# Performance work log

Measured on AMD Instinct MI355X. Metric: run time of the kernel, lower is better.

Reference implementation:

```python
import jax, jax.numpy as jnp
import numpy as np

N_HEAD = 16
D_HEAD = 64
MAX_REL = 512  # max_relative_positions


def setup_inputs() -> dict:
    key = jax.random.key(0)
    ks = jax.random.split(key, 9)
    B, S, D = 2, 2048, 1024
    return {
        "hidden_states": jax.random.normal(ks[0], (B, S, D), jnp.float32),
        "Wq": jax.random.normal(ks[1], (D, D), jnp.float32) * 0.02,
        "bq": jnp.zeros((D,), jnp.float32),
        "Wk": jax.random.normal(ks[2], (D, D), jnp.float32) * 0.02,
        "bk": jnp.zeros((D,), jnp.float32),
        "Wv": jax.random.normal(ks[3], (D, D), jnp.float32) * 0.02,
        "bv": jnp.zeros((D,), jnp.float32),
        "Wc": jax.random.normal(ks[4], (D, D), jnp.float32) * 0.02,
        "pos_table": jax.random.normal(ks[5], (2 * MAX_REL, D_HEAD), jnp.float32) * 0.02,
    }


def reference(hidden_states, Wq, bq, Wk, bk, Wv, bv, Wc, pos_table):
    B, S, D = hidden_states.shape
    H, Dh = N_HEAD, D_HEAD

    # QKV projections (torch Linear: x @ W.T + b)
    q = hidden_states @ Wq.T + bq
    k = hidden_states @ Wk.T + bk
    v = hidden_states @ Wv.T + bv
    q = q.reshape(B, S, H, Dh).transpose(0, 2, 1, 3)  # b h s d
    k = k.reshape(B, S, H, Dh).transpose(0, 2, 1, 3)
    v = v.reshape(B, S, H, Dh).transpose(0, 2, 1, 3)

    # relative position embedding lookup: [S, S, Dh]
    ar = jnp.arange(S)
    rel = jnp.clip(ar[:, None] - ar[None, :] + MAX_REL, 0, 2 * MAX_REL - 1)
    rpe = pos_table[rel]  # (S, S, Dh)

    # c2p: original einsum 'bhld,ijd->bhij' sums q over l (faithful)
    c2p = jnp.einsum('bhld,ijd->bhij', q, rpe)
    p2c = jnp.einsum('bhjd,ijd->bhij', k, jnp.flip(rpe, axis=0))
    bias = c2p + p2c  # (B, H, S, S)

    # SDPA with explicit attn_mask == bias added to scaled scores
    scale = 1.0 / jnp.sqrt(jnp.asarray(Dh, hidden_states.dtype))
    scores = jnp.einsum('bhid,bhjd->bhij', q, k) * scale + bias
    attn = jax.nn.softmax(scores, axis=-1)
    out = jnp.einsum('bhij,bhjd->bhid', attn, v)  # (B, H, S, Dh)

    out = out.transpose(0, 2, 1, 3).reshape(B, S, D)
    return out @ Wc.T  # c_proj has no bias; dropout is identity in eval
```

## Files before the change

kernel.cpp:

```cpp
#include <hip/hip_runtime.h>
#include <math.h>

#define BN   2
#define SEQ  2048
#define DIM  1024
#define NH   16
#define DH   64
#define TAB  1024
#define SCALE 0.125f
#define LOG2E 1.44269504088896340736f

typedef __attribute__((ext_vector_type(8))) short bf16x8;
typedef __attribute__((ext_vector_type(4))) float f32x4;

#if defined(__has_builtin)
#if __has_builtin(__builtin_amdgcn_exp2f)
#define EXP2F(x) __builtin_amdgcn_exp2f(x)
#else
#define EXP2F(x) exp2f(x)
#endif
#else
#define EXP2F(x) exp2f(x)
#endif

__device__ __forceinline__ short f2b(float f) {
    union { float f; unsigned u; } x; x.f = f;
    return (short)((x.u + 0x7fffu + ((x.u >> 16) & 1u)) >> 16);
}
__device__ __forceinline__ float b2f(short s) {
    union { float f; unsigned u; } x; x.u = ((unsigned)(unsigned short)s) << 16;
    return x.f;
}

#define GLDS16(gp, lp) __builtin_amdgcn_global_load_lds( \
    (const __attribute__((address_space(1))) void*)(gp), \
    (__attribute__((address_space(3))) void*)(lp), 16, 0, 0)

__device__ __forceinline__ bf16x8 fragS(const short* base, int row, int kq) {
    return *(const bf16x8*)(base + row * 64 + ((kq ^ (row & 7)) << 3));
}

__global__ __launch_bounds__(256) void f2b_multi_kernel(
    const float* __restrict__ s0, short* __restrict__ d0, int n0,
    const float* __restrict__ s1, short* __restrict__ d1,
    const float* __restrict__ s2, short* __restrict__ d2,
    const float* __restrict__ s3, short* __restrict__ d3, int nw,
    const float* __restrict__ s4, short* __restrict__ d4, int n4)
{
    const int z = blockIdx.z;
    const float* src = z == 0 ? s0 : (z == 1 ? s1 : (z == 2 ? s2 : (z == 3 ? s3 : s4)));
    short* dst       = z == 0 ? d0 : (z == 1 ? d1 : (z == 2 ? d2 : (z == 3 ? d3 : d4)));
    const int n      = z == 0 ? n0 : (z == 4 ? n4 : nw);
    int i = (blockIdx.x * 256 + threadIdx.x) * 8;
    if (i >= n) return;
    float4 a = *(const float4*)&src[i];
    float4 b = *(const float4*)&src[i + 4];
    bf16x8 o = { f2b(a.x), f2b(a.y), f2b(a.z), f2b(a.w),
                 f2b(b.x), f2b(b.y), f2b(b.z), f2b(b.w) };
    *(bf16x8*)&dst[i] = o;
}

__global__ __launch_bounds__(256) void qkv_mfma_kernel(
    const short* __restrict__ xb,
    const short* __restrict__ Wqb, const float* __restrict__ bq,
    const short* __restrict__ Wkb, const float* __restrict__ bk,
    const short* __restrict__ Wvb, const float* __restrict__ bv,
    short* __restrict__ q, short* __restrict__ k, short* __restrict__ v)
{
    const int which = blockIdx.z;
    const short* W    = which == 0 ? Wqb : (which == 1 ? Wkb : Wvb);
    const float* bias = which == 0 ? bq  : (which == 1 ? bk  : bv);
    short* outp       = which == 0 ? q   : (which == 1 ? k   : v);
    const float osc   = which == 0 ? SCALE * LOG2E : 1.0f;

    const int m0 = blockIdx.y * 128;
    const int n0 = blockIdx.x * 128;

    __shared__ short As[128 * 64];
    __shared__ short Bs[128 * 64];

    const int t  = threadIdx.x;
    const int w  = t >> 6;
    const int q4 = (t >> 4) & 3;
    const int l  = t & 15;
    const int wm = (w >> 1) * 64;
    const int wn = (w & 1) * 64;

    f32x4 acc[4][4];
#pragma unroll
    for (int mt = 0; mt < 4; ++mt)
#pragma unroll
        for (int nt = 0; nt < 4; ++nt) acc[mt][nt] = (f32x4){0.f,0.f,0.f,0.f};

    for (int k0 = 0; k0 < DIM; k0 += 64) {
        __syncthreads();
#pragma unroll
        for (int p = 0; p < 4; ++p) {
            const int cq = p * 256 + t;
            const int row = cq >> 3, bd = cq & 7;
            const int goff = (bd ^ (row & 7)) << 3;
            GLDS16(xb + (size_t)(m0 + row) * DIM + k0 + goff, As + cq * 8);
            GLDS16(W  + (size_t)(n0 + row) * DIM + k0 + goff, Bs + cq * 8);
        }
        __syncthreads();
#pragma unroll
        for (int kc = 0; kc < 2; ++kc) {
            bf16x8 af[4], bf[4];
#pragma unroll
            for (int mt = 0; mt < 4; ++mt) af[mt] = fragS(As, wm + mt*16 + l, kc*4 + q4);
#pragma unroll
            for (int nt = 0; nt < 4; ++nt) bf[nt] = fragS(Bs, wn + nt*16 + l, kc*4 + q4);
#pragma unroll
            for (int mt = 0; mt < 4; ++mt)
#pragma unroll
                for (int nt = 0; nt < 4; ++nt)
                    acc[mt][nt] = __builtin_amdgcn_mfma_f32_16x16x32_bf16(
                        af[mt], bf[nt], acc[mt][nt], 0, 0, 0);
        }
    }

    float bv4[4];
#pragma unroll
    for (int nt = 0; nt < 4; ++nt) bv4[nt] = bias[n0 + wn + nt*16 + l];
#pragma unroll
    for (int mt = 0; mt < 4; ++mt) {
#pragma unroll
        for (int r = 0; r < 4; ++r) {
            const int m  = m0 + wm + mt*16 + q4*4 + r;
            const int b_ = m >> 11, s_ = m & 2047;
#pragma unroll
            for (int nt = 0; nt < 4; ++nt) {
                const int o  = n0 + wn + nt*16 + l;
                const int h_ = o >> 6, d_ = o & 63;
                outp[((size_t)(b_*NH + h_) * SEQ + s_) * DH + d_] =
                    f2b((acc[mt][nt][r] + bv4[nt]) * osc);
            }
        }
    }
}

__global__ __launch_bounds__(256) void qsum_c2p_kernel(
    const short* __restrict__ q, const float* __restrict__ pt, float* __restrict__ c2p)
{
    const int bh = blockIdx.x;
    const short* qb = q + (size_t)bh * SEQ * DH;
    __shared__ float part[32][72];
    __shared__ float qs[64];
    const int t = threadIdx.x;
    const int dg = t & 7, sc = t >> 3;
    float a[8];
#pragma unroll
    for (int c = 0; c < 8; ++c) a[c] = 0.f;
    for (int s = sc * 64; s < sc * 64 + 64; ++s) {
        bf16x8 vv = *(const bf16x8*)&qb[(size_t)s * DH + dg * 8];
#pragma unroll
        for (int c = 0; c < 8; ++c) a[c] += b2f(vv[c]);
    }
#pragma unroll
    for (int c = 0; c < 8; ++c) part[sc][dg*8 + c] = a[c];
    __syncthreads();
    if (t < 64) {
        float s = 0.f;
#pragma unroll 8
        for (int i = 0; i < 32; ++i) s += part[i][t];
        qs[t] = s * 8.0f;
    }
    __syncthreads();
    for (int c = t; c < TAB; c += 256) {
        const float* ptr = pt + (size_t)c * DH;
        float s = 0.f;
#pragma unroll
        for (int dd = 0; dd < DH; dd += 4) {
            float4 p4 = *(const float4*)&ptr[dd];
            s += qs[dd]*p4.x + qs[dd+1]*p4.y + qs[dd+2]*p4.z + qs[dd+3]*p4.w;
        }
        c2p[(size_t)bh * TAB + c] = s;
    }
}

__global__ __launch_bounds__(256) void tgemm_kernel(
    const short* __restrict__ kglob, const short* __restrict__ ptb,
    short* __restrict__ slab, int bh0)
{
    const int G    = gridDim.z;
    const int gsub = G >> 3;
    const int fid  = (blockIdx.z * gridDim.y + blockIdx.y) * gridDim.x + blockIdx.x;
    const int g    = (fid & 7) * gsub + ((fid >> 3) % gsub);
    const int rest = fid / (8 * gsub);
    const int m0 = (rest >> 3) * 128;
    const int n0 = (rest & 7) * 128;

    const int bh = bh0 + g;
    const short* A = kglob + (size_t)bh * SEQ * DH;

    __shared__ short As[128 * 64];
    __shared__ short Bs[128 * 64];

    const int t  = threadIdx.x;
    const int w  = t >> 6;
    const int q4 = (t >> 4) & 3;
    const int l  = t & 15;
    const int wm = (w >> 1) * 64;
    const int wn = (w & 1) * 64;

#pragma unroll
    for (int p = 0; p < 4; ++p) {
        const int cq = p * 256 + t;
        const int row = cq >> 3, bd = cq & 7;
        const int go = (bd ^ (row & 7)) << 3;
        GLDS16(A   + (size_t)(m0 + row) * DH + go, As + cq * 8);
        GLDS16(ptb + (size_t)(n0 + row) * DH + go, Bs + cq * 8);
    }
    __syncthreads();

    f32x4 acc[4][4];
#pragma unroll
    for (int mt = 0; mt < 4; ++mt)
#pragma unroll
        for (int nt = 0; nt < 4; ++nt) acc[mt][nt] = (f32x4){0.f,0.f,0.f,0.f};
#pragma unroll
    for (int kc = 0; kc < 2; ++kc) {
        bf16x8 af[4], bf[4];
#pragma unroll
        for (int mt = 0; mt < 4; ++mt) af[mt] = fragS(As, wm + mt*16 + l, kc*4 + q4);
#pragma unroll
        for (int nt = 0; nt < 4; ++nt) bf[nt] = fragS(Bs, wn + nt*16 + l, kc*4 + q4);
#pragma unroll
        for (int mt = 0; mt < 4; ++mt)
#pragma unroll
            for (int nt = 0; nt < 4; ++nt)
                acc[mt][nt] = __builtin_amdgcn_mfma_f32_16x16x32_bf16(
                    af[mt], bf[nt], acc[mt][nt], 0, 0, 0);
    }

    short* outp = slab + (size_t)g * SEQ * 1024;
#pragma unroll
    for (int mt = 0; mt < 4; ++mt)
#pragma unroll
        for (int r = 0; r < 4; ++r) {
            const int m = m0 + wm + mt*16 + q4*4 + r;
#pragma unroll
            for (int nt = 0; nt < 4; ++nt)
                outp[(size_t)m * 1024 + n0 + wn + nt*16 + l] =
                    f2b(acc[mt][nt][r] * LOG2E);
        }
}

__global__ __launch_bounds__(256, 3) void attn_kernel(
    const short* __restrict__ q, const short* __restrict__ k, const short* __restrict__ v,
    const float* __restrict__ c2p, const short* __restrict__ slab,
    short* __restrict__ ao, int bh0)
{
    const int G    = gridDim.y;
    const int gsub = G >> 3;
    const int fid  = blockIdx.y * gridDim.x + blockIdx.x;
    const int g    = (fid & 7) * gsub + ((fid >> 3) % gsub);
    const int i0   = (fid / (8 * gsub)) * 64;

    const int bh = bh0 + g;
    const int b_ = bh >> 4, h_ = bh & 15;
    const short* qbh = q + (size_t)bh * SEQ * DH;
    const short* kbh = k + (size_t)bh * SEQ * DH;
    const short* vbh = v + (size_t)bh * SEQ * DH;
    const float* c2pb = c2p + (size_t)bh * TAB;
    const short* Tb   = slab + (size_t)g * SEQ * 1024;

    __shared__ short Ks[64 * 64];
    __shared__ short Vt[64 * 64];

    const int t    = threadIdx.x;
    const int w    = t >> 6;
    const int q4   = (t >> 4) & 3;
    const int l    = t & 15;
    const int iLoc = w*16 + l;
    const int pq   = ((q4 & 1) << 1) | (q4 >> 1);

    const int jp  = t & 31;
    const int dgv = t >> 5;

#pragma unroll
    for (int p = 0; p < 2; ++p) {
        const int cq = p * 256 + t;
        const int row = cq >> 3, bd = cq & 7;
        GLDS16(qbh + (size_t)(i0 + row) * DH + ((bd ^ (row & 7)) << 3), Ks + cq * 8);
    }
    __syncthreads();
    const bf16x8 aq0 = fragS(Ks, w*16 + l, q4);
    const bf16x8 aq1 = fragS(Ks, w*16 + l, 4 + q4);
    __syncthreads();

    float lsum = 0.f;
    f32x4 O[4];
#pragma unroll
    for (int dt = 0; dt < 4; ++dt) O[dt] = (f32x4){0.f, 0.f, 0.f, 0.f};

    for (int j0 = 0; j0 < SEQ; j0 += 64) {
        const int Kc0 = 2559 - i0 - j0;

#pragma unroll
        for (int p = 0; p < 2; ++p) {
            const int cq = p * 256 + t;
            const int row = cq >> 3, bd = cq & 7;
            GLDS16(kbh + (size_t)(j0 + row) * DH + ((bd ^ (row & 7)) << 3), Ks + cq * 8);
        }
        {
            const int j = 2 * jp, d0 = dgv * 8;
            bf16x8 va = *(const bf16x8*)(vbh + (size_t)(j0 + j)     * DH + d0);
            bf16x8 vb = *(const bf16x8*)(vbh + (size_t)(j0 + j + 1) * DH + d0);
#pragma unroll
            for (int c = 0; c < 8; ++c) {
                const int d = d0 + c;
                const int slot = d * 64 + (((j >> 3) ^ (d & 7)) << 3) + (j & 7);
                short2 pr; pr.x = va[c]; pr.y = vb[c];
                *(short2*)&Vt[slot] = pr;
            }
        }
        __syncthreads();

        f32x4 st4[4];
        const int ccb = 512 + i0 + iLoc - j0;
#pragma unroll
        for (int jt = 0; jt < 4; ++jt)
#pragma unroll
            for (int r = 0; r < 4; ++r) {
                const int jl = jt*16 + q4*4 + r;
                st4[jt][r] = c2pb[min(max(ccb - jl, 0), TAB - 1)];
            }

        short tband[16];
#pragma unroll
        for (int jt = 0; jt < 4; ++jt)
#pragma unroll
            for (int r = 0; r < 4; ++r) {
                const int jl = jt*16 + q4*4 + r;
                const int y  = min(max(Kc0 - jl - iLoc, 0), TAB - 1);
                tband[jt*4 + r] = Tb[(size_t)(j0 + jl) * 1024 + y];
            }

        __builtin_amdgcn_s_setprio(1);
#pragma unroll
        for (int jt = 0; jt < 4; ++jt) {
            bf16x8 a0 = fragS(Ks, jt*16 + l, q4);
            bf16x8 a1 = fragS(Ks, jt*16 + l, 4 + q4);
            st4[jt] = __builtin_amdgcn_mfma_f32_16x16x32_bf16(a0, aq0, st4[jt], 0, 0, 0);
            st4[jt] = __builtin_amdgcn_mfma_f32_16x16x32_bf16(a1, aq1, st4[jt], 0, 0, 0);
        }
        __builtin_amdgcn_s_setprio(0);

        float pv4[4][4];
#pragma unroll
        for (int jt = 0; jt < 4; ++jt)
#pragma unroll
            for (int r = 0; r < 4; ++r) {
                pv4[jt][r] = EXP2F(st4[jt][r] + b2f(tband[jt*4 + r]));
                lsum += pv4[jt][r];
            }

        unsigned P2[4][2];
#pragma unroll
        for (int t2 = 0; t2 < 4; ++t2) {
            asm("v_cvt_pk_bf16_f32 %0, %1, %2"
                : "=v"(P2[t2][0]) : "v"(pv4[t2][0]), "v"(pv4[t2][1]));
            asm("v_cvt_pk_bf16_f32 %0, %1, %2"
                : "=v"(P2[t2][1]) : "v"(pv4[t2][2]), "v"(pv4[t2][3]));
        }
#pragma unroll
        for (int m = 0; m < 2; ++m) {
            asm("v_permlane16_swap_b32 %0, %1" : "+v"(P2[0][m]), "+v"(P2[1][m]));
            asm("v_permlane16_swap_b32 %0, %1" : "+v"(P2[2][m]), "+v"(P2[3][m]));
        }
        union { unsigned u[4]; bf16x8 v8; } UA, UB;
        UA.u[0] = P2[0][0]; UA.u[1] = P2[0][1]; UA.u[2] = P2[1][0]; UA.u[3] = P2[1][1];
        UB.u[0] = P2[2][0]; UB.u[1] = P2[2][1]; UB.u[2] = P2[3][0]; UB.u[3] = P2[3][1];

        __builtin_amdgcn_s_setprio(1);
#pragma unroll
        for (int dt = 0; dt < 4; ++dt) {
            bf16x8 b0 = fragS(Vt, dt*16 + l, pq);
            bf16x8 b1 = fragS(Vt, dt*16 + l, 4 + pq);
            O[dt] = __builtin_amdgcn_mfma_f32_16x16x32_bf16(UA.v8, b0, O[dt], 0, 0, 0);
            O[dt] = __builtin_amdgcn_mfma_f32_16x16x32_bf16(UB.v8, b1, O[dt], 0, 0, 0);
        }
        __builtin_amdgcn_s_setprio(0);
        __syncthreads();
    }

    lsum += __shfl_xor(lsum, 16);
    lsum += __shfl_xor(lsum, 32);

#pragma unroll
    for (int r = 0; r < 4; ++r) {
        const float inv = 1.f / __shfl(lsum, q4*4 + r);
        const int i_g = i0 + w*16 + q4*4 + r;
        short* dst = ao + (((size_t)b_ * SEQ + i_g) * NH + h_) * DH + l;
#pragma unroll
        for (int dt = 0; dt < 4; ++dt)
            dst[dt*16] = f2b(O[dt][r] * inv);
    }
}

__global__ __launch_bounds__(256) void out_mfma_kernel(
    const short* __restrict__ xb, const float* __restrict__ W, float* __restrict__ out)
{
    const int m0 = blockIdx.y * 128;
    const int n0 = blockIdx.x * 128;

    __shared__ short As[128 * 64];
    __shared__ short Bs[128 * 64];

    const int t  = threadIdx.x;
    const int w  = t >> 6;
    const int q4 = (t >> 4) & 3;
    const int l  = t & 15;
    const int wm = (w >> 1) * 64;
    const int wn = (w & 1) * 64;

    f32x4 acc[4][4];
#pragma unroll
    for (int mt = 0; mt < 4; ++mt)
#pragma unroll
        for (int nt = 0; nt < 4; ++nt) acc[mt][nt] = (f32x4){0.f,0.f,0.f,0.f};

    for (int k0 = 0; k0 < DIM; k0 += 64) {
        __syncthreads();
#pragma unroll
        for (int p = 0; p < 4; ++p) {
            const int cq = p * 256 + t;
            const int row = cq >> 3, bd = cq & 7;
            GLDS16(xb + (size_t)(m0 + row) * DIM + k0 + ((bd ^ (row & 7)) << 3), As + cq * 8);
        }
        {
            const int row = t >> 1, h = t & 1;
#pragma unroll
            for (int c = 0; c < 4; ++c) {
                const int gch = h * 4 + c;
                const float* src = W + (size_t)(n0 + row) * DIM + k0 + gch * 8;
                float4 f0 = *(const float4*)src;
                float4 f1 = *(const float4*)(src + 4);
                bf16x8 o = { f2b(f0.x), f2b(f0.y), f2b(f0.z), f2b(f0.w),
                             f2b(f1.x), f2b(f1.y), f2b(f1.z), f2b(f1.w) };
                *(bf16x8*)&Bs[row * 64 + ((gch ^ (row & 7)) << 3)] = o;
            }
        }
        __syncthreads();
#pragma unroll
        for (int kc = 0; kc < 2; ++kc) {
            bf16x8 af[4], bf[4];
#pragma unroll
            for (int mt = 0; mt < 4; ++mt) af[mt] = fragS(As, wm + mt*16 + l, kc*4 + q4);
#pragma unroll
            for (int nt = 0; nt < 4; ++nt) bf[nt] = fragS(Bs, wn + nt*16 + l, kc*4 + q4);
#pragma unroll
            for (int mt = 0; mt < 4; ++mt)
#pragma unroll
                for (int nt = 0; nt < 4; ++nt)
                    acc[mt][nt] = __builtin_amdgcn_mfma_f32_16x16x32_bf16(
                        af[mt], bf[nt], acc[mt][nt], 0, 0, 0);
        }
    }
#pragma unroll
    for (int mt = 0; mt < 4; ++mt)
#pragma unroll
        for (int r = 0; r < 4; ++r) {
            const int m = m0 + wm + mt*16 + q4*4 + r;
#pragma unroll
            for (int nt = 0; nt < 4; ++nt)
                out[(size_t)m * DIM + n0 + wn + nt*16 + l] = acc[mt][nt][r];
        }
}

extern "C" void kernel_launch(void* const* d_in, const int* in_sizes, int n_in,
                              void* d_out, int out_size, void* d_ws, size_t ws_size,
                              hipStream_t stream)
{
    const float* hs = (const float*)d_in[0];
    const float* Wq = (const float*)d_in[1];
    const float* bq = (const float*)d_in[2];
    const float* Wk = (const float*)d_in[3];
    const float* bk = (const float*)d_in[4];
    const float* Wv = (const float*)d_in[5];
    const float* bv = (const float*)d_in[6];
    const float* Wc = (const float*)d_in[7];
    const float* pt = (const float*)d_in[8];
    float* out = (float*)d_out;

    const size_t XE    = (size_t)BN * SEQ * DIM;
    const size_t WE    = (size_t)DIM * DIM;
    const size_t PE    = (size_t)TAB * DH;
    const size_t SLAB1 = (size_t)SEQ * 1024;

    short* sw   = (short*)d_ws;
    short* qb   = sw;
    short* kb   = sw + XE;
    short* vb   = sw + 2 * XE;
    short* aob  = sw + 3 * XE;
    float* c2p  = (float*)(sw + 4 * XE);
    short* ptb  = sw + 4 * XE + 65536;
    short* slab = sw + 4 * XE + 65536 + PE;
    short* xb   = slab;
    short* wqb  = slab + XE;
    short* wkb  = wqb + WE;
    short* wvb  = wkb + WE;

    const size_t fixed_sh = 4 * XE + 65536 + PE;
    const size_t avail_sh = (ws_size / 2 > fixed_sh) ? ws_size / 2 - fixed_sh : 0;
    const int G = (avail_sh >= 32 * SLAB1) ? 32 : ((avail_sh >= 16 * SLAB1) ? 16 : 8);

    f2b_multi_kernel<<<dim3((int)(XE/2048), 1, 5), 256, 0, stream>>>(
        hs, xb, (int)XE, Wq, wqb, Wk, wkb, Wv, wvb, (int)WE, pt, ptb, (int)PE);

    qkv_mfma_kernel<<<dim3(DIM/128, (BN*SEQ)/128, 3), 256, 0, stream>>>(
        xb, wqb, bq, wkb, bk, wvb, bv, qb, kb, vb);

    qsum_c2p_kernel<<<dim3(BN*NH), 256, 0, stream>>>(qb, pt, c2p);

    for (int bh0 = 0; bh0 < BN*NH; bh0 += G) {
        tgemm_kernel<<<dim3(1024/128, SEQ/128, G), 256, 0, stream>>>(kb, ptb, slab, bh0);
        attn_kernel<<<dim3(SEQ/64, G), 256, 0, stream>>>(qb, kb, vb, c2p, slab, aob, bh0);
    }

    out_mfma_kernel<<<dim3(DIM/128, (BN*SEQ)/128), 256, 0, stream>>>(aob, Wc, out);
}
```

Before: 308.9 us.

## Double-buffer K/V tiles in attention loop and raise occupancy hint to 4

The attention kernel now keeps two shared-memory buffers each for K and transposed V. The next tile is loaded while the current one is computed, which cuts one barrier per iteration and hides global load latency. The launch bounds also rise from 3 to 4 blocks per SM. This doubles LDS use to 32KB per block and may cause register pressure or spills under the tighter occupancy hint.

New measurement: 313.8 us. About the same (+1.6%).

```diff
diff --git a/kernel.cpp b/kernel.cpp
--- a/kernel.cpp
+++ b/kernel.cpp
@@ -246,7 +246,7 @@
         }
 }
 
-__global__ __launch_bounds__(256, 3) void attn_kernel(
+__global__ __launch_bounds__(256, 4) void attn_kernel(
     const short* __restrict__ q, const short* __restrict__ k, const short* __restrict__ v,
     const float* __restrict__ c2p, const short* __restrict__ slab,
     short* __restrict__ ao, int bh0)
@@ -265,8 +265,8 @@
     const float* c2pb = c2p + (size_t)bh * TAB;
     const short* Tb   = slab + (size_t)g * SEQ * 1024;
 
-    __shared__ short Ks[64 * 64];
-    __shared__ short Vt[64 * 64];
+    __shared__ short KsA[64 * 64], KsB[64 * 64];
+    __shared__ short VtA[64 * 64], VtB[64 * 64];
 
     const int t    = threadIdx.x;
     const int w    = t >> 6;
@@ -282,40 +282,66 @@
     for (int p = 0; p < 2; ++p) {
         const int cq = p * 256 + t;
         const int row = cq >> 3, bd = cq & 7;
-        GLDS16(qbh + (size_t)(i0 + row) * DH + ((bd ^ (row & 7)) << 3), Ks + cq * 8);
+        GLDS16(qbh + (size_t)(i0 + row) * DH + ((bd ^ (row & 7)) << 3), KsA + cq * 8);
     }
     __syncthreads();
-    const bf16x8 aq0 = fragS(Ks, w*16 + l, q4);
-    const bf16x8 aq1 = fragS(Ks, w*16 + l, 4 + q4);
+    const bf16x8 aq0 = fragS(KsA, w*16 + l, q4);
+    const bf16x8 aq1 = fragS(KsA, w*16 + l, 4 + q4);
     __syncthreads();
 
-    float lsum = 0.f;
-    f32x4 O[4];
-#pragma unroll
-    for (int dt = 0; dt < 4; ++dt) O[dt] = (f32x4){0.f, 0.f, 0.f, 0.f};
-
-    for (int j0 = 0; j0 < SEQ; j0 += 64) {
-        const int Kc0 = 2559 - i0 - j0;
-
+    {
 #pragma unroll
         for (int p = 0; p < 2; ++p) {
             const int cq = p * 256 + t;
             const int row = cq >> 3, bd = cq & 7;
-            GLDS16(kbh + (size_t)(j0 + row) * DH + ((bd ^ (row & 7)) << 3), Ks + cq * 8);
-        }
-        {
+            GLDS16(kbh + (size_t)row * DH + ((bd ^ (row & 7)) << 3), KsA + cq * 8);
+        }
+        const int j = 2 * jp, d0 = dgv * 8;
+        bf16x8 va = *(const bf16x8*)(vbh + (size_t)j       * DH + d0);
+        bf16x8 vb = *(const bf16x8*)(vbh + (size_t)(j + 1) * DH + d0);
+#pragma unroll
+        for (int c = 0; c < 8; ++c) {
+            const int d = d0 + c;
+            const int slot = d * 64 + (((j >> 3) ^ (d & 7)) << 3) + (j & 7);
+            short2 pr; pr.x = va[c]; pr.y = vb[c];
+            *(short2*)&VtA[slot] = pr;
+        }
+    }
+    __syncthreads();
+
+    float lsum = 0.f;
+    f32x4 O[4];
+#pragma unroll
+    for (int dt = 0; dt < 4; ++dt) O[dt] = (f32x4){0.f, 0.f, 0.f, 0.f};
+
+    for (int it = 0; it < 32; ++it) {
+        const int j0  = it * 64;
+        const int Kc0 = 2559 - i0 - j0;
+        const int par = it & 1;
+        const short* KsC = par ? KsB : KsA;
+        const short* VtC = par ? VtB : VtA;
+        short* KsN = par ? KsA : KsB;
+        short* VtN = par ? VtA : VtB;
+
+        if (it < 31) {
+            const int j0n = j0 + 64;
+#pragma unroll
+            for (int p = 0; p < 2; ++p) {
+                const int cq = p * 256 + t;
+                const int row = cq >> 3, bd = cq & 7;
+                GLDS16(kbh + (size_t)(j0n + row) * DH + ((bd ^ (row & 7)) << 3), KsN + cq * 8);
+            }
             const int j = 2 * jp, d0 = dgv * 8;
-            bf16x8 va = *(const bf16x8*)(vbh + (size_t)(j0 + j)     * DH + d0);
-            bf16x8 vb = *(const bf16x8*)(vbh + (size_t)(j0 + j + 1) * DH + d0);
+            bf16x8 va = *(const bf16x8*)(vbh + (size_t)(j0n + j)     * DH + d0);
+            bf16x8 vb = *(const bf16x8*)(vbh + (size_t)(j0n + j + 1) * DH + d0);
 #pragma unroll
             for (int c = 0; c < 8; ++c) {
                 const int d = d0 + c;
                 const int slot = d * 64 + (((j >> 3) ^ (d & 7)) << 3) + (j & 7);
                 short2 pr; pr.x = va[c]; pr.y = vb[c];
-                *(short2*)&Vt[slot] = pr;
-            }
-        }
-        __syncthreads();
+                *(short2*)&VtN[slot] = pr;
+            }
+        }
 
         f32x4 st4[4];
         const int ccb = 512 + i0 + iLoc - j0;
@@ -340,8 +366,8 @@
         __builtin_amdgcn_s_setprio(1);
 #pragma unroll
         for (int jt = 0; jt < 4; ++jt) {
-            bf16x8 a0 = fragS(Ks, jt*16 + l, q4);
-            bf16x8 a1 = fragS(Ks, jt*16 + l, 4 + q4);
+            bf16x8 a0 = fragS(KsC, jt*16 + l, q4);
+            bf16x8 a1 = fragS(KsC, jt*16 + l, 4 + q4);
             st4[jt] = __builtin_amdgcn_mfma_f32_16x16x32_bf16(a0, aq0, st4[jt], 0, 0, 0);
             st4[jt] = __builtin_amdgcn_mfma_f32_16x16x32_bf16(a1, aq1, st4[jt], 0, 0, 0);
         }
@@ -376,12 +402,13 @@
         __builtin_amdgcn_s_setprio(1);
 #pragma unroll
         for (int dt = 0; dt < 4; ++dt) {
-            bf16x8 b0 = fragS(Vt, dt*16 + l, pq);
-            bf16x8 b1 = fragS(Vt, dt*16 + l, 4 + pq);
+            bf16x8 b0 = fragS(VtC, dt*16 + l, pq);
+            bf16x8 b1 = fragS(VtC, dt*16 + l, 4 + pq);
             O[dt] = __builtin_amdgcn_mfma_f32_16x16x32_bf16(UA.v8, b0, O[dt], 0, 0, 0);
             O[dt] = __builtin_amdgcn_mfma_f32_16x16x32_bf16(UB.v8, b1, O[dt], 0, 0, 0);
         }
         __builtin_amdgcn_s_setprio(0);
+
         __syncthreads();
     }
 
```
